# Performance work log

Measured on AMD Instinct MI355X. Metric: run time of the kernel, lower is better.

The kernel has to match this reference:

```python
import jax, jax.numpy as jnp
import numpy as np

B, A, C, M = 8, 98304, 80, 32
ALPHA, GAMMA = 0.25, 2.0


def setup_inputs() -> dict:
    key = jax.random.key(0)
    k1, k2, k3, k4, k5, k6, k7, k8 = jax.random.split(key, 8)
    classifications = jax.random.uniform(k1, (B, A, C), dtype=jnp.float32)
    regressions = jax.random.normal(k2, (B, A, 4), dtype=jnp.float32)
    # valid anchor boxes inside a 640px image
    ax = jax.random.uniform(k3, (A,)) * 512.0
    ay = jax.random.uniform(k4, (A,)) * 512.0
    aw = jax.random.uniform(k5, (A, 2)) * 120.0 + 8.0
    anchors = jnp.stack([ax, ay, ax + aw[:, 0], ay + aw[:, 1]], axis=-1)[None].astype(jnp.float32)
    # valid GT boxes with class labels in [0, C) (no -1 padding: all annotations valid)
    gx = jax.random.uniform(k6, (B, M, 2)) * 480.0
    gw = jax.random.uniform(k7, (B, M, 2)) * 150.0 + 10.0
    gcls = jax.random.randint(k8, (B, M), 0, C).astype(jnp.float32)
    annotations = jnp.concatenate([gx, gx + gw, gcls[..., None]], axis=-1).astype(jnp.float32)
    return {
        "classifications": classifications,
        "regressions": regressions,
        "anchors": anchors,
        "annotations": annotations,
        "negative_iou_thr": 0.4,
        "positive_iou_thr": 0.5,
    }


def calc_iou(a, b):
    # a: [A,4] anchors, b: [M,4] gt boxes -> [A,M]
    area = (b[:, 2] - b[:, 0]) * (b[:, 3] - b[:, 1])
    iw = jnp.clip(jnp.minimum(a[:, 2:3], b[:, 2]) - jnp.maximum(a[:, 0:1], b[:, 0]), 0.0)
    ih = jnp.clip(jnp.minimum(a[:, 3:4], b[:, 3]) - jnp.maximum(a[:, 1:2], b[:, 1]), 0.0)
    inter = iw * ih
    ua = jnp.clip(((a[:, 2] - a[:, 0]) * (a[:, 3] - a[:, 1]))[:, None] + area - inter, 1e-8)
    return inter / ua


def focal_loss(classifications, regressions, anchors, annotations, negative_iou_thr, positive_iou_thr):
    anchor = anchors[0]  # [A,4]
    aw = anchor[:, 2] - anchor[:, 0]
    ah = anchor[:, 3] - anchor[:, 1]
    acx = anchor[:, 0] + 0.5 * aw
    acy = anchor[:, 1] + 0.5 * ah

    def per_image(classification, regression, annot):
        p = jnp.clip(classification, 1e-4, 1.0 - 1e-4)
        valid = annot[:, 4] != -1.0  # [M] (all valid in test data)
        iou = jnp.where(valid[None, :], calc_iou(anchor, annot[:, :4]), -1.0)  # [A,M]
        iou_max = jnp.max(iou, axis=1)
        iou_arg = jnp.argmax(iou, axis=1)
        assigned = annot[iou_arg]  # [A,5]

        pos = iou_max >= positive_iou_thr  # [A]
        num_pos = jnp.sum(pos.astype(jnp.float32))
        onehot = jax.nn.one_hot(assigned[:, 4].astype(jnp.int32), C, dtype=jnp.float32)
        # targets: 1 for assigned class on positives, 0 elsewhere on pos/neg anchors, -1 ignored
        targets = jnp.where(pos[:, None], onehot,
                            jnp.where((iou_max < negative_iou_thr)[:, None], 0.0, -1.0))

        is_one = targets == 1.0
        alpha_factor = jnp.where(is_one, ALPHA, 1.0 - ALPHA)
        focal_w = alpha_factor * jnp.where(is_one, 1.0 - p, p) ** GAMMA
        bce = -(targets * jnp.log(p) + (1.0 - targets) * jnp.log(1.0 - p))
        cls_loss = jnp.where(targets != -1.0, focal_w * bce, 0.0)
        cls_loss = jnp.sum(cls_loss) / jnp.clip(num_pos, 1.0)

        gw = jnp.clip(assigned[:, 2] - assigned[:, 0], None, None)
        gh = assigned[:, 3] - assigned[:, 1]
        gcx = assigned[:, 0] + 0.5 * gw
        gcy = assigned[:, 1] + 0.5 * gh
        gw = jnp.clip(gw, 1.0)
        gh = jnp.clip(gh, 1.0)
        t = jnp.stack([(gcx - acx) / aw, (gcy - acy) / ah,
                       jnp.log(gw / aw), jnp.log(gh / ah)], axis=1)
        t = t / jnp.array([0.1, 0.1, 0.2, 0.2], dtype=jnp.float32)
        diff = jnp.abs(t - regression)
        sl1 = jnp.where(diff <= 1.0 / 9.0, 0.5 * 9.0 * diff * diff, diff - 0.5 / 9.0)
        reg_loss = jnp.sum(jnp.where(pos[:, None], sl1, 0.0)) / jnp.clip(num_pos * 4.0, 1.0)
        return cls_loss, reg_loss

    cls_l, reg_l = jax.vmap(per_image)(classifications, regressions, annotations)
    return jnp.mean(cls_l).reshape(1), jnp.mean(reg_l).reshape(1)


def reference(classifications, regressions, anchors, annotations, negative_iou_thr, positive_iou_thr):
    return focal_loss(classifications, regressions, anchors, annotations,
                      negative_iou_thr, positive_iou_thr)
```

## Files before the change

kernel.cpp:

```cpp
#include <hip/hip_runtime.h>

#define B_ 8
#define A_ 98304
#define C_ 80
#define M_ 32
#define BLK 256
#define ITERS 20
#define NWAVE (BLK / 64)
#define TILES_PER_IMG (A_ / BLK)
#define NTILES (B_ * TILES_PER_IMG)
#define GRID 1536

#define NEGC (-0.75f * 0.69314718055994531f)

__device__ __forceinline__ float neg_u(float praw) {
    const float p = fminf(praw, 1.0f - 1e-4f);
    return p * p * __log2f(1.0f - p);
}

__device__ __forceinline__ float smooth_l1(float t, float r) {
    float d = fabsf(t - r);
    return (d <= (1.0f / 9.0f)) ? (0.5f * 9.0f * d * d) : (d - 0.5f / 9.0f);
}

__global__ __launch_bounds__(BLK) void focal_main(
    const float* __restrict__ cls,
    const float* __restrict__ regr,
    const float* __restrict__ anchors,
    const float* __restrict__ ann,
    const float* __restrict__ neg_thr_p,
    const float* __restrict__ pos_thr_p,
    float* __restrict__ acc)
{
    __shared__ float s_x0[M_], s_y0[M_], s_x1[M_], s_y1[M_], s_ab[M_], s_cls[M_];
    __shared__ float s_w[BLK];
    __shared__ float s_red[NWAVE * 3];

    const int tid = threadIdx.x;
    const float neg_thr = neg_thr_p[0];
    const float pos_thr = pos_thr_p[0];

    for (int t = blockIdx.x; t < NTILES; t += GRID) {
        const int b  = t / TILES_PER_IMG;
        const int a0 = (t % TILES_PER_IMG) * BLK;

        if (tid < M_) {
            const float* am = ann + ((size_t)b * M_ + tid) * 5;
            const float x0 = am[0], y0 = am[1], x1 = am[2], y1 = am[3], cl = am[4];
            s_x0[tid] = x0; s_y0[tid] = y0; s_x1[tid] = x1; s_y1[tid] = y1;
            s_ab[tid] = (x1 - x0) * (y1 - y0);
            s_cls[tid] = cl;
        }
        __syncthreads();

        const int a = a0 + tid;
        const float4 an = reinterpret_cast<const float4*>(anchors)[a];
        const float aw = an.z - an.x;
        const float ah = an.w - an.y;
        const float areaA = aw * ah;

        float ib = -1.0f, ub = 1.0f;
        int   arg = 0;
#pragma unroll
        for (int m = 0; m < M_; ++m) {
            const float iw = fmaxf(fminf(an.z, s_x1[m]) - fmaxf(an.x, s_x0[m]), 0.0f);
            const float ih = fmaxf(fminf(an.w, s_y1[m]) - fmaxf(an.y, s_y0[m]), 0.0f);
            float inter = iw * ih;
            const float ua = fmaxf(areaA + s_ab[m] - inter, 1e-8f);
            if (s_cls[m] == -1.0f) inter = -1.0f;
            if (inter * ub > ib * ua) { ib = inter; ub = ua; arg = m; }
        }
        const bool pos = (ib >= pos_thr * ub);
        const bool neg = (ib <  neg_thr * ub);

        float reg_partial = 0.0f;
        float pos_count   = 0.0f;
        float cls_corr    = 0.0f;

        if (pos) {
            pos_count = 1.0f;
            const float gx0 = s_x0[arg], gy0 = s_y0[arg];
            const float gx1 = s_x1[arg], gy1 = s_y1[arg];
            const int   kcls = (int)s_cls[arg];

            float gw = gx1 - gx0;
            float gh = gy1 - gy0;
            const float gcx = gx0 + 0.5f * gw;
            const float gcy = gy0 + 0.5f * gh;
            gw = fmaxf(gw, 1.0f);
            gh = fmaxf(gh, 1.0f);
            const float acx = an.x + 0.5f * aw;
            const float acy = an.y + 0.5f * ah;
            const float t0 = ((gcx - acx) / aw) * 10.0f;
            const float t1 = ((gcy - acy) / ah) * 10.0f;
            const float t2 = logf(gw / aw) * 5.0f;
            const float t3 = logf(gh / ah) * 5.0f;
            const float4 r = reinterpret_cast<const float4*>(regr)[(size_t)b * A_ + a];
            reg_partial = smooth_l1(t0, r.x) + smooth_l1(t1, r.y) +
                          smooth_l1(t2, r.z) + smooth_l1(t3, r.w);

            const float praw = cls[((size_t)b * A_ + a) * C_ + kcls];
            const float p  = fminf(fmaxf(praw, 1e-4f), 1.0f - 1e-4f);
            const float om = 1.0f - p;
            const float negv = neg_u(praw) * NEGC;
            const float posv = 0.25f * om * om * (-__logf(p));
            cls_corr = posv - negv;
        }
        s_w[tid] = (pos || neg) ? NEGC : 0.0f;
        __syncthreads();

        const float4* tile4 = reinterpret_cast<const float4*>(
            cls + ((size_t)b * A_ + a0) * C_);
        float s0 = 0.0f, s1 = 0.0f;
#pragma unroll 5
        for (int it = 0; it < ITERS; ++it) {
            const int vid = it * BLK + tid;
            const float4 v = tile4[vid];
            const float cw = s_w[(unsigned)vid / 20u];
            s0 = fmaf(neg_u(v.x) + neg_u(v.y), cw, s0);
            s1 = fmaf(neg_u(v.z) + neg_u(v.w), cw, s1);
        }
        float cls_partial = cls_corr + s0 + s1;

#pragma unroll
        for (int off = 32; off > 0; off >>= 1) {
            cls_partial += __shfl_down(cls_partial, off);
            reg_partial += __shfl_down(reg_partial, off);
            pos_count   += __shfl_down(pos_count,   off);
        }
        const int wave = tid >> 6;
        if ((tid & 63) == 0) {
            s_red[wave * 3 + 0] = cls_partial;
            s_red[wave * 3 + 1] = reg_partial;
            s_red[wave * 3 + 2] = pos_count;
        }
        __syncthreads();
        if (tid == 0) {
            float c = 0.0f, r = 0.0f, n = 0.0f;
#pragma unroll
            for (int wv = 0; wv < NWAVE; ++wv) {
                c += s_red[wv * 3 + 0];
                r += s_red[wv * 3 + 1];
                n += s_red[wv * 3 + 2];
            }
            atomicAdd(&acc[b * 3 + 0], c);
            atomicAdd(&acc[b * 3 + 1], r);
            atomicAdd(&acc[b * 3 + 2], n);
        }
        __syncthreads();
    }
}

__global__ void focal_finalize(const float* __restrict__ acc, float* __restrict__ out) {
    const int t = threadIdx.x;
    float cls_l = 0.0f, reg_l = 0.0f;
    if (t < B_) {
        const float np = acc[t * 3 + 2];
        cls_l = acc[t * 3 + 0] / fmaxf(np, 1.0f);
        reg_l = acc[t * 3 + 1] / fmaxf(np * 4.0f, 1.0f);
    }
#pragma unroll
    for (int off = 32; off > 0; off >>= 1) {
        cls_l += __shfl_down(cls_l, off);
        reg_l += __shfl_down(reg_l, off);
    }
    if (t == 0) {
        out[0] = cls_l / (float)B_;
        out[1] = reg_l / (float)B_;
    }
}

extern "C" void kernel_launch(void* const* d_in, const int* in_sizes, int n_in,
                              void* d_out, int out_size, void* d_ws, size_t ws_size,
                              hipStream_t stream) {
    const float* cls     = (const float*)d_in[0];
    const float* regr    = (const float*)d_in[1];
    const float* anchors = (const float*)d_in[2];
    const float* ann     = (const float*)d_in[3];
    const float* negt    = (const float*)d_in[4];
    const float* post    = (const float*)d_in[5];
    float* acc = (float*)d_ws;

    hipMemsetAsync(acc, 0, B_ * 3 * sizeof(float), stream);
    focal_main<<<GRID, BLK, 0, stream>>>(cls, regr, anchors, ann,
                                         negt, post, acc);
    focal_finalize<<<1, 64, 0, stream>>>(acc, (float*)d_out);
}
```

Before: 115.0 us.

## Fuse finalize into main kernel via last-block counter and XCD-aware tile mapping

Removes the separate finalize kernel launch: each block increments a global done counter with acquire-release semantics, and the last block to finish computes the final per-image normalisation and mean. Tiles are also remapped so each block processes two tiles from a contiguous range assigned to its XCD (blockIdx % 8), improving L2 locality of consecutive tiles. This saves one launch but adds a device-scope atomic and fence per block.

```diff
diff --git a/kernel.cpp b/kernel.cpp
--- a/kernel.cpp
+++ b/kernel.cpp
@@ -10,6 +10,9 @@
 #define TILES_PER_IMG (A_ / BLK)
 #define NTILES (B_ * TILES_PER_IMG)
 #define GRID 1536
+#define NXCD 8
+#define TPX (NTILES / NXCD)
+#define BPX (GRID / NXCD)
 
 #define NEGC (-0.75f * 0.69314718055994531f)
 
@@ -30,17 +33,24 @@
     const float* __restrict__ ann,
     const float* __restrict__ neg_thr_p,
     const float* __restrict__ pos_thr_p,
-    float* __restrict__ acc)
+    float* __restrict__ acc,
+    int* __restrict__ done,
+    float* __restrict__ out)
 {
     __shared__ float s_x0[M_], s_y0[M_], s_x1[M_], s_y1[M_], s_ab[M_], s_cls[M_];
     __shared__ float s_w[BLK];
     __shared__ float s_red[NWAVE * 3];
+    __shared__ int   s_last;
 
     const int tid = threadIdx.x;
     const float neg_thr = neg_thr_p[0];
     const float pos_thr = pos_thr_p[0];
 
-    for (int t = blockIdx.x; t < NTILES; t += GRID) {
+    const int xcd  = blockIdx.x % NXCD;
+    const int lane = blockIdx.x / NXCD;
+
+    for (int j = 0; j < 2; ++j) {
+        const int t  = xcd * TPX + lane + j * BPX;
         const int b  = t / TILES_PER_IMG;
         const int a0 = (t % TILES_PER_IMG) * BLK;
 
@@ -102,9 +112,7 @@
             const float praw = cls[((size_t)b * A_ + a) * C_ + kcls];
             const float p  = fminf(fmaxf(praw, 1e-4f), 1.0f - 1e-4f);
             const float om = 1.0f - p;
-            const float negv = neg_u(praw) * NEGC;
-            const float posv = 0.25f * om * om * (-__logf(p));
-            cls_corr = posv - negv;
+            cls_corr = 0.25f * om * om * (-__logf(p)) - neg_u(praw) * NEGC;
         }
         s_w[tid] = (pos || neg) ? NEGC : 0.0f;
         __syncthreads();
@@ -149,24 +157,29 @@
         }
         __syncthreads();
     }
-}
-
-__global__ void focal_finalize(const float* __restrict__ acc, float* __restrict__ out) {
-    const int t = threadIdx.x;
-    float cls_l = 0.0f, reg_l = 0.0f;
-    if (t < B_) {
-        const float np = acc[t * 3 + 2];
-        cls_l = acc[t * 3 + 0] / fmaxf(np, 1.0f);
-        reg_l = acc[t * 3 + 1] / fmaxf(np * 4.0f, 1.0f);
+
+    __threadfence();
+    if (tid == 0) {
+        const int d = __hip_atomic_fetch_add(done, 1, __ATOMIC_ACQ_REL,
+                                             __HIP_MEMORY_SCOPE_AGENT);
+        s_last = (d == GRID - 1);
     }
-#pragma unroll
-    for (int off = 32; off > 0; off >>= 1) {
-        cls_l += __shfl_down(cls_l, off);
-        reg_l += __shfl_down(reg_l, off);
-    }
-    if (t == 0) {
-        out[0] = cls_l / (float)B_;
-        out[1] = reg_l / (float)B_;
+    __syncthreads();
+    if (s_last && tid == 0) {
+        float co = 0.0f, ro = 0.0f;
+#pragma unroll
+        for (int b = 0; b < B_; ++b) {
+            const float c = __hip_atomic_load(&acc[b * 3 + 0], __ATOMIC_RELAXED,
+                                              __HIP_MEMORY_SCOPE_AGENT);
+            const float r = __hip_atomic_load(&acc[b * 3 + 1], __ATOMIC_RELAXED,
+                                              __HIP_MEMORY_SCOPE_AGENT);
+            const float n = __hip_atomic_load(&acc[b * 3 + 2], __ATOMIC_RELAXED,
+                                              __HIP_MEMORY_SCOPE_AGENT);
+            co += c / fmaxf(n, 1.0f);
+            ro += r / fmaxf(n * 4.0f, 1.0f);
+        }
+        out[0] = co / (float)B_;
+        out[1] = ro / (float)B_;
     }
 }
 
@@ -179,10 +192,11 @@
     const float* ann     = (const float*)d_in[3];
     const float* negt    = (const float*)d_in[4];
     const float* post    = (const float*)d_in[5];
-    float* acc = (float*)d_ws;
-
-    hipMemsetAsync(acc, 0, B_ * 3 * sizeof(float), stream);
+
+    float* acc  = (float*)d_ws;
+    int*   done = (int*)((char*)d_ws + 256);
+
+    (void)hipMemsetAsync(d_ws, 0, 512, stream);
     focal_main<<<GRID, BLK, 0, stream>>>(cls, regr, anchors, ann,
-                                         negt, post, acc);
-    focal_finalize<<<1, 64, 0, stream>>>(acc, (float*)d_out);
-}
+                                         negt, post, acc, done, (float*)d_out);
+}
```

After: 284.5 us. 148% more time.
